# Performance work log

Hardware: AMD Instinct MI355X
Metric: run time of the kernel (lower is better)

Reference implementation:

```python
import jax, jax.numpy as jnp
import numpy as np
from jax.ops import segment_sum

B = 4096      # graphs per side (= batch of triples)
NPG = 32      # nodes per graph
N = B * NPG   # total nodes per batched graph
EPG = 128     # edges per graph
E = B * EPG   # total edges per batched graph
D = 256       # emb_dim
D4 = D // 4   # gnn1 out dim


def setup_inputs() -> dict:
    key = jax.random.key(0)
    ks = jax.random.split(key, 16)
    base = jnp.repeat(jnp.arange(B, dtype=jnp.int32) * NPG, EPG)  # graph offsets per edge
    def edges(k1, k2):
        s = base + jax.random.randint(k1, (E,), 0, NPG, dtype=jnp.int32)
        d = base + jax.random.randint(k2, (E,), 0, NPG, dtype=jnp.int32)
        return s, d
    subj_src, subj_dst = edges(ks[0], ks[1])
    obj_src, obj_dst = edges(ks[2], ks[3])
    node_graph_ids = jnp.repeat(jnp.arange(B, dtype=jnp.int32), NPG)
    # negative sampling indices (precomputed randomness, as in _sample_batch_negative_triples)
    head_or_tail = jax.random.randint(ks[4], (B,), 0, 2, dtype=jnp.int32)
    random_rows = jax.random.permutation(ks[5], B).astype(jnp.int32)
    ar = jnp.arange(B, dtype=jnp.int32)
    corrupt_hidx = jnp.where(head_or_tail == 1, random_rows, ar)
    corrupt_tidx = jnp.where(head_or_tail == 0, random_rows, ar)
    s = 0.02
    p = lambda k, sh: jax.random.normal(k, sh, dtype=jnp.float32) * s
    return {
        "subj_node_embs": jax.random.normal(ks[6], (N, D), dtype=jnp.float32),
        "obj_node_embs": jax.random.normal(ks[7], (N, D), dtype=jnp.float32),
        "rel_tok_embs": jax.random.normal(ks[8], (B, D), dtype=jnp.float32),
        "subj_src": subj_src, "subj_dst": subj_dst,
        "obj_src": obj_src, "obj_dst": obj_dst,
        "node_graph_ids": node_graph_ids,
        "corrupt_hidx": corrupt_hidx, "corrupt_tidx": corrupt_tidx,
        "WO1": p(ks[9], (D4, D)), "bO1": jnp.zeros((D4,), jnp.float32),
        "WI1": p(ks[10], (D4, D)), "bI1": jnp.zeros((D4,), jnp.float32),
        "WO2": p(ks[11], (D, D4)), "bO2": jnp.zeros((D,), jnp.float32),
        "WI2": p(ks[12], (D, D4)), "bI2": jnp.zeros((D,), jnp.float32),
        "relW": p(ks[13], (D, D)), "relb": jnp.zeros((D,), jnp.float32),
    }


def _mean_agg(h, idx_from, idx_to, n):
    # mean over edges (idx_from -> idx_to) of h[idx_from], per destination node; 0 for isolated
    deg = segment_sum(jnp.ones((idx_from.shape[0],), h.dtype), idx_to, num_segments=n)
    s = segment_sum(jnp.take(h, idx_from, axis=0), idx_to, num_segments=n)
    return s / jnp.maximum(deg, 1.0)[:, None]


def _compgcn(src, dst, h, WO, bO, WI, bI):
    n = h.shape[0]
    ho = _mean_agg(h, src, dst, n)   # forward graph: mean of in-neighbor sources
    hi = _mean_agg(h, dst, src, n)   # reversed graph: mean of out-neighbor targets
    return (ho @ WO.T + bO) + (hi @ WI.T + bI)


def _graph_emb(src, dst, node_embs, gids, WO1, bO1, WI1, bI1, WO2, bO2, WI2, bI2):
    hn = jax.nn.relu(_compgcn(src, dst, node_embs, WO1, bO1, WI1, bI1))
    hn = jax.nn.relu(_compgcn(src, dst, hn, WO2, bO2, WI2, bI2))
    # mean readout per graph
    cnt = segment_sum(jnp.ones((hn.shape[0],), hn.dtype), gids, num_segments=B)
    return segment_sum(hn, gids, num_segments=B) / cnt[:, None]


def _dist(h, r, t):
    return jnp.linalg.norm(h + r - t, ord=2, axis=1)


def reference(subj_node_embs, obj_node_embs, rel_tok_embs,
              subj_src, subj_dst, obj_src, obj_dst, node_graph_ids,
              corrupt_hidx, corrupt_tidx,
              WO1, bO1, WI1, bI1, WO2, bO2, WI2, bI2, relW, relb):
    h_embs = _graph_emb(subj_src, subj_dst, subj_node_embs, node_graph_ids,
                        WO1, bO1, WI1, bI1, WO2, bO2, WI2, bI2)
    t_embs = _graph_emb(obj_src, obj_dst, obj_node_embs, node_graph_ids,
                        WO1, bO1, WI1, bI1, WO2, bO2, WI2, bI2)
    r_embs = jax.nn.relu(rel_tok_embs @ relW.T + relb)
    pos_scores = _dist(h_embs, r_embs, t_embs)
    neg_scores = _dist(h_embs[corrupt_hidx], r_embs, t_embs[corrupt_tidx])
    return pos_scores, neg_scores
```

## Files before the change

### kernel.cpp

```cpp
#include <hip/hip_runtime.h>
#include <hip/hip_bf16.h>

#define BGR 4096
#define DIM 256
#define NG  16
#define HS  257

#define OFF_EB 0
#define OFF_H1 0
#define OFF_A2 4608
#define OFF_YT 16896
#define OFF_CW 27136

typedef __bf16 bf16x8 __attribute__((ext_vector_type(8)));
typedef __bf16 bf16x4 __attribute__((ext_vector_type(4)));
typedef float  f32x4  __attribute__((ext_vector_type(4)));

__device__ __forceinline__ unsigned short f2b(float f) {
  unsigned u = __builtin_bit_cast(unsigned, f);
  u = (u + 0x7FFFu + ((u >> 16) & 1u)) >> 16;
  return (unsigned short)u;
}

__device__ __forceinline__ bf16x4 cvt4(f32x4 c) {
  bf16x4 r;
  r[0] = (__bf16)c[0]; r[1] = (__bf16)c[1]; r[2] = (__bf16)c[2]; r[3] = (__bf16)c[3];
  return r;
}

__device__ __forceinline__ void lds_barrier() {
  asm volatile("s_waitcnt lgkmcnt(0)" ::: "memory");
  __builtin_amdgcn_s_barrier();
  __builtin_amdgcn_sched_barrier(0);
}

__global__ void wcvt_kernel(
    const float* __restrict__ WO1, const float* __restrict__ WI1,
    const float* __restrict__ WO2, const float* __restrict__ WI2,
    const float* __restrict__ bO1, const float* __restrict__ bI1,
    const float* __restrict__ bO2, const float* __restrict__ bI2,
    unsigned short* __restrict__ W1b, unsigned short* __restrict__ W2b,
    float* __restrict__ b1, float* __restrict__ b2)
{
  const int i = blockIdx.x * 256 + threadIdx.x;
  { int j = i >> 8, k = i & 255;
    float v = (j < 64) ? WO1[j * 256 + k] : WI1[(j - 64) * 256 + k];
    W1b[i] = f2b(v); }
  { int j = i >> 7, k = i & 127;
    float v = (k < 64) ? WO2[j * 64 + k] : WI2[j * 64 + (k - 64)];
    W2b[i] = f2b(v); }
  if (i < 64)  b1[i] = bO1[i] + bI1[i];
  if (i < 256) b2[i] = bO2[i] + bI2[i];
}

__global__ __launch_bounds__(256)
__attribute__((amdgpu_waves_per_eu(1, 2)))
void fused_kernel(
    const float* __restrict__ subj, const float* __restrict__ obj,
    const int* __restrict__ ssrc, const int* __restrict__ sdst,
    const int* __restrict__ osrc, const int* __restrict__ odst,
    const unsigned short* __restrict__ W1b, const unsigned short* __restrict__ W2b,
    const float* __restrict__ b1, const float* __restrict__ b2,
    float* __restrict__ gout)
{
  __shared__ __align__(16) unsigned char S[29696];
  const int t = threadIdx.x, w = t >> 6, l = t & 63;
  const int ln16 = l & 15, kg = l >> 4;
  const int gid0 = blockIdx.x * NG;

  float4 ev[8];
  {
    const int gid = gid0;
    const float* Eg = ((gid >> 12) ? obj : subj) + (size_t)(gid & (BGR - 1)) * 32 * DIM;
    #pragma unroll
    for (int i = 0; i < 8; i++)
      ev[i] = *(const float4*)(Eg + (w * 8 + i) * 256 + l * 4);
  }
  int es = 0, ed = 0;
  if (t < 128) {
    const int gid = gid0, g = gid & (BGR - 1);
    es = (((gid >> 12) ? osrc : ssrc))[g * 128 + t] & 31;
    ed = (((gid >> 12) ? odst : sdst))[g * 128 + t] & 31;
  }
  bf16x8 B0[8], B1[8];
  {
    const unsigned short* wb0 = W1b + ((2 * w) * 16 + ln16) * 256 + kg * 8;
    const unsigned short* wb1 = W1b + ((2 * w + 1) * 16 + ln16) * 256 + kg * 8;
    #pragma unroll
    for (int ks = 0; ks < 8; ks++) {
      B0[ks] = *(const bf16x8*)(wb0 + ks * 32);
      B1[ks] = *(const bf16x8*)(wb1 + ks * 32);
    }
  }
  bf16x8 AW[4][4];
  float4 b2v[4];
  #pragma unroll
  for (int q = 0; q < 4; q++) {
    const int mt = w * 4 + q;
    const unsigned short* wa = W2b + (mt * 16 + ln16) * 128 + kg * 8;
    #pragma unroll
    for (int ks = 0; ks < 4; ks++) AW[q][ks] = *(const bf16x8*)(wa + ks * 32);
    b2v[q] = *(const float4*)(b2 + mt * 16 + kg * 4);
  }
  const float b1j = b1[w * 16 + ln16];
  {
    unsigned* cw = (unsigned*)(S + OFF_CW);
    for (int i = t; i < 640; i += 256) cw[i] = 0;
  }
  __syncthreads();
  if (t < 128) {
    unsigned* cw = (unsigned*)(S + OFF_CW);
    atomicAdd(&cw[ed * 8 + (es >> 2)], 1u << ((es & 3) * 8));
    atomicAdd(&cw[256 + ed], 1u);
    atomicAdd(&cw[288 + es], 1u);
  }

  for (int g = 0; g < NG; g++) {
    const int gid = gid0 + g;
    unsigned* cwc = (unsigned*)(S + OFF_CW + (g & 1) * 1280);
    unsigned* cwn = (unsigned*)(S + OFF_CW + ((g + 1) & 1) * 1280);

    #pragma unroll
    for (int i = 0; i < 8; i++) {
      f32x4 tmp = {ev[i].x, ev[i].y, ev[i].z, ev[i].w};
      *(bf16x4*)(S + OFF_EB + (w * 8 + i) * 528 + l * 8) = cvt4(tmp);
    }
    if (g + 1 < NG) {
      for (int i = t; i < 320; i += 256) cwn[i] = 0;
      const int ngid = gid + 1, ngg = ngid & (BGR - 1);
      const float* Eg = ((ngid >> 12) ? obj : subj) + (size_t)ngg * 32 * DIM;
      #pragma unroll
      for (int i = 0; i < 8; i++)
        ev[i] = *(const float4*)(Eg + (w * 8 + i) * 256 + l * 4);
      if (t < 128) {
        es = (((ngid >> 12) ? osrc : ssrc))[ngg * 128 + t] & 31;
        ed = (((ngid >> 12) ? odst : sdst))[ngg * 128 + t] & 31;
      }
    }
    lds_barrier();

    {
      f32x4 a00 = {0,0,0,0}, a01 = {0,0,0,0}, a10 = {0,0,0,0}, a11 = {0,0,0,0};
      const unsigned char* ea = S + OFF_EB + ln16 * 528 + kg * 16;
      #pragma unroll
      for (int ks = 0; ks < 8; ks++) {
        bf16x8 A0 = *(const bf16x8*)(ea + ks * 64);
        bf16x8 A1 = *(const bf16x8*)(ea + 16 * 528 + ks * 64);
        a00 = __builtin_amdgcn_mfma_f32_16x16x32_bf16(A0, B0[ks], a00, 0, 0, 0);
        a01 = __builtin_amdgcn_mfma_f32_16x16x32_bf16(A0, B1[ks], a01, 0, 0, 0);
        a10 = __builtin_amdgcn_mfma_f32_16x16x32_bf16(A1, B0[ks], a10, 0, 0, 0);
        a11 = __builtin_amdgcn_mfma_f32_16x16x32_bf16(A1, B1[ks], a11, 0, 0, 0);
      }
      *(bf16x4*)(S + OFF_YT + ((2 * w) * 16 + ln16) * 80 + (kg * 4) * 2)          = cvt4(a00);
      *(bf16x4*)(S + OFF_YT + ((2 * w + 1) * 16 + ln16) * 80 + (kg * 4) * 2)      = cvt4(a01);
      *(bf16x4*)(S + OFF_YT + ((2 * w) * 16 + ln16) * 80 + (16 + kg * 4) * 2)     = cvt4(a10);
      *(bf16x4*)(S + OFF_YT + ((2 * w + 1) * 16 + ln16) * 80 + (16 + kg * 4) * 2) = cvt4(a11);
    }
    lds_barrier();

    if (g + 1 < NG && t < 128) {
      atomicAdd(&cwn[ed * 8 + (es >> 2)], 1u << ((es & 3) * 8));
      atomicAdd(&cwn[256 + ed], 1u);
      atomicAdd(&cwn[288 + es], 1u);
    }

    bf16x8 m1f[2], m2f[2];
    #pragma unroll
    for (int hf = 0; hf < 2; hf++) {
      const int r = hf * 16 + ln16;
      const float fi = 1.0f / fmaxf((float)cwc[256 + r], 1.0f);
      const float fo = 1.0f / fmaxf((float)cwc[288 + r], 1.0f);
      const unsigned w0 = cwc[r * 8 + kg * 2], w1 = cwc[r * 8 + kg * 2 + 1];
      bf16x8 a, b;
      #pragma unroll
      for (int q = 0; q < 4; q++) {
        a[q]     = (__bf16)((float)((w0 >> (q * 8)) & 255u) * fi);
        a[4 + q] = (__bf16)((float)((w1 >> (q * 8)) & 255u) * fi);
      }
      #pragma unroll
      for (int q = 0; q < 8; q++) {
        const unsigned wq = cwc[(kg * 8 + q) * 8 + (r >> 2)];
        b[q] = (__bf16)((float)((wq >> ((r & 3) * 8)) & 255u) * fo);
      }
      m1f[hf] = a; m2f[hf] = b;
    }
    {
      bf16x8 Byo = *(const bf16x8*)(S + OFF_YT + (w * 16 + ln16) * 80 + kg * 16);
      bf16x8 Byi = *(const bf16x8*)(S + OFF_YT + (64 + w * 16 + ln16) * 80 + kg * 16);
      #pragma unroll
      for (int mt = 0; mt < 2; mt++) {
        f32x4 z = {0.f, 0.f, 0.f, 0.f};
        f32x4 c = __builtin_amdgcn_mfma_f32_16x16x32_bf16(m1f[mt], Byo, z, 0, 0, 0);
        c = __builtin_amdgcn_mfma_f32_16x16x32_bf16(m2f[mt], Byi, c, 0, 0, 0);
        f32x4 hv = { fmaxf(c[0] + b1j, 0.f), fmaxf(c[1] + b1j, 0.f),
                     fmaxf(c[2] + b1j, 0.f), fmaxf(c[3] + b1j, 0.f) };
        *(bf16x4*)(S + OFF_H1 + (w * 16 + ln16) * 72 + (mt * 16 + kg * 4) * 2) = cvt4(hv);
      }
    }

    {
      bf16x8 Af = *(const bf16x8*)(S + OFF_H1 + (w * 16 + ln16) * 72 + kg * 16);
      #pragma unroll
      for (int hf = 0; hf < 2; hf++)
        #pragma unroll
        for (int ntd = 0; ntd < 2; ntd++) {
          f32x4 z = {0.f, 0.f, 0.f, 0.f};
          f32x4 c = __builtin_amdgcn_mfma_f32_16x16x32_bf16(
              Af, hf ? m2f[ntd] : m1f[ntd], z, 0, 0, 0);
          *(bf16x4*)(S + OFF_A2 + (ntd * 16 + ln16) * 272 + hf * 128 + w * 32 + kg * 8) = cvt4(c);
        }
    }
    lds_barrier();

    {
      bf16x8 BF[2][4];
      #pragma unroll
      for (int ntd = 0; ntd < 2; ntd++)
        #pragma unroll
        for (int ks = 0; ks < 4; ks++)
          BF[ntd][ks] = *(const bf16x8*)(S + OFF_A2 + (ntd * 16 + ln16) * 272 + ks * 64 + kg * 16);
      #pragma unroll
      for (int q = 0; q < 4; q++) {
        const int mt = w * 4 + q;
        f32x4 a0 = {0.f, 0.f, 0.f, 0.f}, a1 = {0.f, 0.f, 0.f, 0.f};
        #pragma unroll
        for (int ks = 0; ks < 4; ks++) {
          a0 = __builtin_amdgcn_mfma_f32_16x16x32_bf16(AW[q][ks], BF[0][ks], a0, 0, 0, 0);
          a1 = __builtin_amdgcn_mfma_f32_16x16x32_bf16(AW[q][ks], BF[1][ks], a1, 0, 0, 0);
        }
        float v0 = fmaxf(a0[0] + b2v[q].x, 0.f) + fmaxf(a1[0] + b2v[q].x, 0.f);
        float v1 = fmaxf(a0[1] + b2v[q].y, 0.f) + fmaxf(a1[1] + b2v[q].y, 0.f);
        float v2 = fmaxf(a0[2] + b2v[q].z, 0.f) + fmaxf(a1[2] + b2v[q].z, 0.f);
        float v3 = fmaxf(a0[3] + b2v[q].w, 0.f) + fmaxf(a1[3] + b2v[q].w, 0.f);
        #pragma unroll
        for (int d = 1; d < 16; d <<= 1) {
          v0 += __shfl_xor(v0, d); v1 += __shfl_xor(v1, d);
          v2 += __shfl_xor(v2, d); v3 += __shfl_xor(v3, d);
        }
        if (ln16 == 0) {
          float4 o = { v0 * 0.03125f, v1 * 0.03125f, v2 * 0.03125f, v3 * 0.03125f };
          *(float4*)(gout + (size_t)gid * DIM + mt * 16 + kg * 4) = o;
        }
      }
    }
    if (g + 1 < NG) lds_barrier();
  }
}

__global__ __launch_bounds__(256, 4) void rel_kernel(
    const float* __restrict__ rel, const float* __restrict__ relW,
    const float* __restrict__ relb, float* __restrict__ r_out)
{
  __shared__ float srel[16 * HS];
  const int t = threadIdx.x;
  const int b0 = blockIdx.x << 4;
  #pragma unroll
  for (int i = 0; i < 4; i++) {
    int f = (i << 8) + t;
    int r = f >> 6, k4 = f & 63;
    float4 x = *(const float4*)(rel + (size_t)(b0 + r) * DIM + (k4 << 2));
    float* d = &srel[r * HS + (k4 << 2)];
    d[0] = x.x; d[1] = x.y; d[2] = x.z; d[3] = x.w;
  }
  __syncthreads();
  const int r = t & 15, jg = t >> 4;
  const float* pa = &srel[r * HS];
  const float* w = relW + (size_t)(jg * 16) * DIM;
  float acc[16];
  #pragma unroll
  for (int jj = 0; jj < 16; jj++) acc[jj] = 0.f;
  for (int k0 = 0; k0 < DIM; k0 += 16) {
    float a[16];
    #pragma unroll
    for (int u = 0; u < 16; u++) a[u] = pa[k0 + u];
    #pragma unroll
    for (int jj = 0; jj < 16; jj++) {
      const float* wr = w + jj * DIM + k0;
      #pragma unroll
      for (int u = 0; u < 16; u += 4) {
        float4 wv = *(const float4*)(wr + u);
        acc[jj] += a[u]*wv.x + a[u+1]*wv.y + a[u+2]*wv.z + a[u+3]*wv.w;
      }
    }
  }
  float* outp = r_out + (size_t)(b0 + r) * DIM + jg * 16;
  #pragma unroll
  for (int jj = 0; jj < 16; jj++) outp[jj] = fmaxf(acc[jj] + relb[jg * 16 + jj], 0.f);
}

__global__ __launch_bounds__(256) void dist_kernel(
    const float* __restrict__ hemb, const float* __restrict__ temb,
    const float* __restrict__ remb, const int* __restrict__ chx,
    const int* __restrict__ ctx, float* __restrict__ out)
{
  const int t = threadIdx.x;
  const int w = t >> 6, l = t & 63;
  const int b = (blockIdx.x << 2) + w;
  float4 h4 = *(const float4*)(hemb + (size_t)b * DIM + (l << 2));
  float4 r4 = *(const float4*)(remb + (size_t)b * DIM + (l << 2));
  float4 t4 = *(const float4*)(temb + (size_t)b * DIM + (l << 2));
  int hb = chx[b], tb = ctx[b];
  float4 hn = *(const float4*)(hemb + (size_t)hb * DIM + (l << 2));
  float4 tn = *(const float4*)(temb + (size_t)tb * DIM + (l << 2));
  float x0 = h4.x + r4.x - t4.x, x1 = h4.y + r4.y - t4.y;
  float x2 = h4.z + r4.z - t4.z, x3 = h4.w + r4.w - t4.w;
  float dp = x0*x0 + x1*x1 + x2*x2 + x3*x3;
  float y0 = hn.x + r4.x - tn.x, y1 = hn.y + r4.y - tn.y;
  float y2 = hn.z + r4.z - tn.z, y3 = hn.w + r4.w - tn.w;
  float dn = y0*y0 + y1*y1 + y2*y2 + y3*y3;
  #pragma unroll
  for (int off = 32; off >= 1; off >>= 1) {
    dp += __shfl_down(dp, off);
    dn += __shfl_down(dn, off);
  }
  if (l == 0) {
    out[b] = sqrtf(dp);
    out[BGR + b] = sqrtf(dn);
  }
}

extern "C" void kernel_launch(void* const* d_in, const int* in_sizes, int n_in,
                              void* d_out, int out_size, void* d_ws, size_t ws_size,
                              hipStream_t stream) {
  const float* subj_embs = (const float*)d_in[0];
  const float* obj_embs  = (const float*)d_in[1];
  const float* rel_tok   = (const float*)d_in[2];
  const int* subj_src = (const int*)d_in[3];
  const int* subj_dst = (const int*)d_in[4];
  const int* obj_src  = (const int*)d_in[5];
  const int* obj_dst  = (const int*)d_in[6];
  const int* chx = (const int*)d_in[8];
  const int* ctx = (const int*)d_in[9];
  const float* WO1 = (const float*)d_in[10];
  const float* bO1 = (const float*)d_in[11];
  const float* WI1 = (const float*)d_in[12];
  const float* bI1 = (const float*)d_in[13];
  const float* WO2 = (const float*)d_in[14];
  const float* bO2 = (const float*)d_in[15];
  const float* WI2 = (const float*)d_in[16];
  const float* bI2 = (const float*)d_in[17];
  const float* relW = (const float*)d_in[18];
  const float* relb = (const float*)d_in[19];

  float* g_embs = (float*)d_ws;
  float* r_embs = g_embs + (size_t)2 * BGR * DIM;
  unsigned short* W1b = (unsigned short*)((char*)d_ws + 12582912);
  unsigned short* W2b = W1b + 32768;
  float* b1 = (float*)((char*)d_ws + 12713984);
  float* b2 = b1 + 64;
  float* out = (float*)d_out;

  wcvt_kernel<<<128, 256, 0, stream>>>(WO1, WI1, WO2, WI2, bO1, bI1, bO2, bI2,
                                       W1b, W2b, b1, b2);
  fused_kernel<<<8192 / NG, 256, 0, stream>>>(
      subj_embs, obj_embs, subj_src, subj_dst, obj_src, obj_dst,
      W1b, W2b, b1, b2, g_embs);
  rel_kernel<<<BGR / 16, 256, 0, stream>>>(rel_tok, relW, relb, r_embs);
  dist_kernel<<<BGR / 4, 256, 0, stream>>>(
      g_embs, g_embs + (size_t)BGR * DIM, r_embs, chx, ctx, out);
}
```

Measured before the change: 199.9 us.

## Deepen graph pipeline: separate LDS regions, drop end-of-iteration barrier, halve graphs per block

Moves the H1/A2 scratch regions out of the region shared with the embedding buffer and YT, so the next graph's embeddings can be converted into LDS during the current graph's second stage. The prefetch now runs two graphs ahead and the trailing barrier per iteration is removed. NG is halved, which doubles the block count, and LDS per block grows, which may lower occupancy. Register pressure from the deeper prefetch may also rise.

```diff
diff --git a/kernel.cpp b/kernel.cpp
--- a/kernel.cpp
+++ b/kernel.cpp
@@ -3,14 +3,14 @@
 
 #define BGR 4096
 #define DIM 256
-#define NG  16
+#define NG  8
 #define HS  257
 
 #define OFF_EB 0
-#define OFF_H1 0
-#define OFF_A2 4608
 #define OFF_YT 16896
-#define OFF_CW 27136
+#define OFF_H1 27136
+#define OFF_A2 31744
+#define OFF_CW 40448
 
 typedef __bf16 bf16x8 __attribute__((ext_vector_type(8)));
 typedef __bf16 bf16x4 __attribute__((ext_vector_type(4)));
@@ -63,24 +63,23 @@
     const float* __restrict__ b1, const float* __restrict__ b2,
     float* __restrict__ gout)
 {
-  __shared__ __align__(16) unsigned char S[29696];
+  __shared__ __align__(16) unsigned char S[43008];
   const int t = threadIdx.x, w = t >> 6, l = t & 63;
   const int ln16 = l & 15, kg = l >> 4;
   const int gid0 = blockIdx.x * NG;
 
   float4 ev[8];
+  int es = 0, ed = 0;
   {
     const int gid = gid0;
     const float* Eg = ((gid >> 12) ? obj : subj) + (size_t)(gid & (BGR - 1)) * 32 * DIM;
     #pragma unroll
     for (int i = 0; i < 8; i++)
       ev[i] = *(const float4*)(Eg + (w * 8 + i) * 256 + l * 4);
-  }
-  int es = 0, ed = 0;
-  if (t < 128) {
-    const int gid = gid0, g = gid & (BGR - 1);
-    es = (((gid >> 12) ? osrc : ssrc))[g * 128 + t] & 31;
-    ed = (((gid >> 12) ? odst : sdst))[g * 128 + t] & 31;
+    if (t < 128) {
+      es = (((gid >> 12) ? osrc : ssrc))[(gid & (BGR - 1)) * 128 + t] & 31;
+      ed = (((gid >> 12) ? odst : sdst))[(gid & (BGR - 1)) * 128 + t] & 31;
+    }
   }
   bf16x8 B0[8], B1[8];
   {
@@ -114,29 +113,27 @@
     atomicAdd(&cw[256 + ed], 1u);
     atomicAdd(&cw[288 + es], 1u);
   }
+  #pragma unroll
+  for (int i = 0; i < 8; i++) {
+    f32x4 tmp = {ev[i].x, ev[i].y, ev[i].z, ev[i].w};
+    *(bf16x4*)(S + OFF_EB + (w * 8 + i) * 528 + l * 8) = cvt4(tmp);
+  }
+  if (NG > 1) {
+    const int gid = gid0 + 1;
+    const float* Eg = ((gid >> 12) ? obj : subj) + (size_t)(gid & (BGR - 1)) * 32 * DIM;
+    #pragma unroll
+    for (int i = 0; i < 8; i++)
+      ev[i] = *(const float4*)(Eg + (w * 8 + i) * 256 + l * 4);
+    if (t < 128) {
+      es = (((gid >> 12) ? osrc : ssrc))[(gid & (BGR - 1)) * 128 + t] & 31;
+      ed = (((gid >> 12) ? odst : sdst))[(gid & (BGR - 1)) * 128 + t] & 31;
+    }
+  }
 
   for (int g = 0; g < NG; g++) {
-    const int gid = gid0 + g;
     unsigned* cwc = (unsigned*)(S + OFF_CW + (g & 1) * 1280);
     unsigned* cwn = (unsigned*)(S + OFF_CW + ((g + 1) & 1) * 1280);
 
-    #pragma unroll
-    for (int i = 0; i < 8; i++) {
-      f32x4 tmp = {ev[i].x, ev[i].y, ev[i].z, ev[i].w};
-      *(bf16x4*)(S + OFF_EB + (w * 8 + i) * 528 + l * 8) = cvt4(tmp);
-    }
-    if (g + 1 < NG) {
-      for (int i = t; i < 320; i += 256) cwn[i] = 0;
-      const int ngid = gid + 1, ngg = ngid & (BGR - 1);
-      const float* Eg = ((ngid >> 12) ? obj : subj) + (size_t)ngg * 32 * DIM;
-      #pragma unroll
-      for (int i = 0; i < 8; i++)
-        ev[i] = *(const float4*)(Eg + (w * 8 + i) * 256 + l * 4);
-      if (t < 128) {
-        es = (((ngid >> 12) ? osrc : ssrc))[ngg * 128 + t] & 31;
-        ed = (((ngid >> 12) ? odst : sdst))[ngg * 128 + t] & 31;
-      }
-    }
     lds_barrier();
 
     {
@@ -155,13 +152,32 @@
       *(bf16x4*)(S + OFF_YT + ((2 * w + 1) * 16 + ln16) * 80 + (kg * 4) * 2)      = cvt4(a01);
       *(bf16x4*)(S + OFF_YT + ((2 * w) * 16 + ln16) * 80 + (16 + kg * 4) * 2)     = cvt4(a10);
       *(bf16x4*)(S + OFF_YT + ((2 * w + 1) * 16 + ln16) * 80 + (16 + kg * 4) * 2) = cvt4(a11);
+      if (g + 1 < NG) for (int i = t; i < 320; i += 256) cwn[i] = 0;
     }
     lds_barrier();
 
-    if (g + 1 < NG && t < 128) {
-      atomicAdd(&cwn[ed * 8 + (es >> 2)], 1u << ((es & 3) * 8));
-      atomicAdd(&cwn[256 + ed], 1u);
-      atomicAdd(&cwn[288 + es], 1u);
+    if (g + 1 < NG) {
+      #pragma unroll
+      for (int i = 0; i < 8; i++) {
+        f32x4 tmp = {ev[i].x, ev[i].y, ev[i].z, ev[i].w};
+        *(bf16x4*)(S + OFF_EB + (w * 8 + i) * 528 + l * 8) = cvt4(tmp);
+      }
+      if (t < 128) {
+        atomicAdd(&cwn[ed * 8 + (es >> 2)], 1u << ((es & 3) * 8));
+        atomicAdd(&cwn[256 + ed], 1u);
+        atomicAdd(&cwn[288 + es], 1u);
+      }
+      if (g + 2 < NG) {
+        const int ngid = gid0 + g + 2, ngg = ngid & (BGR - 1);
+        const float* Eg = ((ngid >> 12) ? obj : subj) + (size_t)ngg * 32 * DIM;
+        #pragma unroll
+        for (int i = 0; i < 8; i++)
+          ev[i] = *(const float4*)(Eg + (w * 8 + i) * 256 + l * 4);
+        if (t < 128) {
+          es = (((ngid >> 12) ? osrc : ssrc))[ngg * 128 + t] & 31;
+          ed = (((ngid >> 12) ? odst : sdst))[ngg * 128 + t] & 31;
+        }
+      }
     }
 
     bf16x8 m1f[2], m2f[2];
@@ -239,11 +255,10 @@
         }
         if (ln16 == 0) {
           float4 o = { v0 * 0.03125f, v1 * 0.03125f, v2 * 0.03125f, v3 * 0.03125f };
-          *(float4*)(gout + (size_t)gid * DIM + mt * 16 + kg * 4) = o;
-        }
-      }
-    }
-    if (g + 1 < NG) lds_barrier();
+          *(float4*)(gout + (size_t)(gid0 + g) * DIM + mt * 16 + kg * 4) = o;
+        }
+      }
+    }
   }
 }
 
```

New measurement: 206.5 us. 1.03x slower.
